# Optimization experiments

Hardware: AMD Instinct MI355X
Metric: run time of the kernel (lower is better)

The kernel has to match this reference:

```python
import jax, jax.numpy as jnp
import numpy as np

B, N, C, D = 1, 8192, 256, 128
MASK_VAL = jnp.float32(-1e16)


def setup_inputs() -> dict:
    key = jax.random.key(0)
    k_in, k_g, k_w, k_b = jax.random.split(key, 4)
    inputs = jax.random.normal(k_in, (B, N, C), dtype=jnp.float32)
    # row has at least one unmasked entry (standard GAT practice).
    graph = (jax.random.uniform(k_g, (N, N)) < 0.01).astype(jnp.float32)
    graph = jnp.maximum(graph, jnp.eye(N, dtype=jnp.float32))
    W = jax.random.normal(k_w, (D, C), dtype=jnp.float32)  # nn.Linear weight [out,in]
    b = jax.random.normal(k_b, (D,), dtype=jnp.float32)
    return {"inputs": inputs, "graph": graph, "W": W, "b": b}


def reference(inputs, graph, W, b):
    # h = W(inputs): [B,N,D]
    h = jnp.einsum('bnc,dc->bnd', inputs, W)
    # dense scores masked by adjacency: [B,N,N]
    scores = jnp.einsum('bnd,bmd->bnm', h, h) * graph[None, :, :]
    # torch: masked_fill_(scores == 0, -1e16)
    scores = jnp.where(scores == 0.0, MASK_VAL, scores)
    attention = jax.nn.softmax(scores, axis=2)
    return jnp.einsum('bnm,bmd->bnd', attention, h) + b
```

## Files before the change

### kernel.cpp

```cpp
#include <hip/hip_runtime.h>
#include <math.h>

#define Nn 8192
#define Cc 256
#define Dd 128
#define CAP 192

typedef float fx4 __attribute__((ext_vector_type(4)));

__global__ __launch_bounds__(256) void wt_kernel(const float* __restrict__ W,
                                                 float4* __restrict__ WT) {
  const int t = blockIdx.x * 256 + threadIdx.x;
  const int c4 = t >> 7;
  const int d  = t & 127;
  const float4 v = *(const float4*)(W + (size_t)d * Cc + c4 * 4);
  WT[c4 * Dd + d] = v;
}

__global__ __launch_bounds__(256) void h_kernel(const float* __restrict__ x,
                                                const float4* __restrict__ WT,
                                                float* __restrict__ h) {
  const int tid = threadIdx.x;
  const int d = tid & 127;
  const int g = tid >> 7;
  const int r0 = blockIdx.x * 16 + g * 8;
  const float4* x4 = (const float4*)(x + (size_t)r0 * Cc);

  float acc[8];
#pragma unroll
  for (int r = 0; r < 8; ++r) acc[r] = 0.f;

#pragma unroll 4
  for (int c4 = 0; c4 < Cc / 4; ++c4) {
    const float4 w = WT[c4 * Dd + d];
#pragma unroll
    for (int r = 0; r < 8; ++r) {
      const float4 u = x4[r * (Cc / 4) + c4];
      acc[r] += u.x * w.x + u.y * w.y + u.z * w.z + u.w * w.w;
    }
  }
#pragma unroll
  for (int r = 0; r < 8; ++r) {
    h[(size_t)(r0 + r) * Dd + d] = acc[r];
  }
}

__global__ __launch_bounds__(256, 4) void gat_fused(const float* __restrict__ graph,
                                                    const float* __restrict__ h,
                                                    const float* __restrict__ bias,
                                                    float* __restrict__ out) {
  __shared__ int idxs[4][CAP];
  const int wv   = threadIdx.x >> 6;
  const int lane = threadIdx.x & 63;
  const int q    = lane >> 4;
  const int ql   = lane & 15;
  const int i = blockIdx.x * 4 + wv;
  int* idx = idxs[wv];

  const float4 hiA = *(const float4*)(h + (size_t)i * Dd + ql * 8);
  const float4 hiB = *(const float4*)(h + (size_t)i * Dd + ql * 8 + 4);

  const fx4* row = (const fx4*)(graph + (size_t)i * Nn);
  const unsigned long long lmask = (1ull << lane) - 1ull;
  int cnt = 0;

  fx4 v[8];
#pragma unroll
  for (int t = 0; t < 8; ++t)
    v[t] = __builtin_nontemporal_load(&row[t * 64 + lane]);

#pragma unroll
  for (int c = 0; c < 4; ++c) {
#pragma unroll
    for (int t = 0; t < 8; ++t) {
      const fx4 cur = v[t];
      if (c < 3)
        v[t] = __builtin_nontemporal_load(&row[(c + 1) * 8 * 64 + t * 64 + lane]);
      const int col = 4 * ((c * 8 + t) * 64 + lane);
      {
        const unsigned long long mk = __ballot(cur.x != 0.f);
        if (mk) {
          const int p = cnt + __popcll(mk & lmask);
          if (cur.x != 0.f && p < CAP) idx[p] = col + 0;
          cnt += __popcll(mk);
        }
      }
      {
        const unsigned long long mk = __ballot(cur.y != 0.f);
        if (mk) {
          const int p = cnt + __popcll(mk & lmask);
          if (cur.y != 0.f && p < CAP) idx[p] = col + 1;
          cnt += __popcll(mk);
        }
      }
      {
        const unsigned long long mk = __ballot(cur.z != 0.f);
        if (mk) {
          const int p = cnt + __popcll(mk & lmask);
          if (cur.z != 0.f && p < CAP) idx[p] = col + 2;
          cnt += __popcll(mk);
        }
      }
      {
        const unsigned long long mk = __ballot(cur.w != 0.f);
        if (mk) {
          const int p = cnt + __popcll(mk & lmask);
          if (cur.w != 0.f && p < CAP) idx[p] = col + 3;
          cnt += __popcll(mk);
        }
      }
    }
  }
  const int m = min(cnt, CAP);

  float M = -INFINITY, L = 0.f;
  float4 accA = {0.f, 0.f, 0.f, 0.f};
  float4 accB = {0.f, 0.f, 0.f, 0.f};

  const int nsteps = (m + 3) >> 2;
  const int nb = (nsteps + 1) >> 1;

  float4 hvA[2], hvB[2];
#pragma unroll
  for (int u = 0; u < 2; ++u) {
    const int e = u * 4 + q;
    const int j = (e < m) ? idx[e] : i;
    hvA[u] = *(const float4*)(h + (size_t)j * Dd + ql * 8);
    hvB[u] = *(const float4*)(h + (size_t)j * Dd + ql * 8 + 4);
  }

  for (int b = 0; b < nb; ++b) {
    float4 nA[2], nB[2];
    if (b + 1 < nb) {
#pragma unroll
      for (int u = 0; u < 2; ++u) {
        const int e = (2 * (b + 1) + u) * 4 + q;
        const int j = (e < m) ? idx[e] : i;
        nA[u] = *(const float4*)(h + (size_t)j * Dd + ql * 8);
        nB[u] = *(const float4*)(h + (size_t)j * Dd + ql * 8 + 4);
      }
    }
    float sv[2];
#pragma unroll
    for (int u = 0; u < 2; ++u) {
      float pd = hiA.x * hvA[u].x + hiA.y * hvA[u].y + hiA.z * hvA[u].z + hiA.w * hvA[u].w
               + hiB.x * hvB[u].x + hiB.y * hvB[u].y + hiB.z * hvB[u].z + hiB.w * hvB[u].w;
#pragma unroll
      for (int off = 8; off > 0; off >>= 1) pd += __shfl_xor(pd, off);
      sv[u] = pd;
    }
#pragma unroll
    for (int u = 0; u < 2; ++u) {
      const int e = (2 * b + u) * 4 + q;
      const float s = (e < m) ? sv[u] : 0.f;
      if (s != 0.f) {
        const float newM = fmaxf(M, s);
        const float scale = __expf(M - newM);
        const float p = __expf(s - newM);
        L = L * scale + p;
        accA.x = accA.x * scale + p * hvA[u].x;
        accA.y = accA.y * scale + p * hvA[u].y;
        accA.z = accA.z * scale + p * hvA[u].z;
        accA.w = accA.w * scale + p * hvA[u].w;
        accB.x = accB.x * scale + p * hvB[u].x;
        accB.y = accB.y * scale + p * hvB[u].y;
        accB.z = accB.z * scale + p * hvB[u].z;
        accB.w = accB.w * scale + p * hvB[u].w;
        M = newM;
      }
    }
#pragma unroll
    for (int u = 0; u < 2; ++u) { hvA[u] = nA[u]; hvB[u] = nB[u]; }
  }

#pragma unroll
  for (int off = 16; off <= 32; off <<= 1) {
    const float Mo = __shfl_xor(M, off);
    const float Lo = __shfl_xor(L, off);
    float4 aAo, aBo;
    aAo.x = __shfl_xor(accA.x, off); aAo.y = __shfl_xor(accA.y, off);
    aAo.z = __shfl_xor(accA.z, off); aAo.w = __shfl_xor(accA.w, off);
    aBo.x = __shfl_xor(accB.x, off); aBo.y = __shfl_xor(accB.y, off);
    aBo.z = __shfl_xor(accB.z, off); aBo.w = __shfl_xor(accB.w, off);
    const float Mm = fmaxf(M, Mo);
    const float s0 = (M  > -INFINITY) ? __expf(M  - Mm) : 0.f;
    const float s1 = (Mo > -INFINITY) ? __expf(Mo - Mm) : 0.f;
    L = L * s0 + Lo * s1;
    accA.x = accA.x * s0 + aAo.x * s1;  accA.y = accA.y * s0 + aAo.y * s1;
    accA.z = accA.z * s0 + aAo.z * s1;  accA.w = accA.w * s0 + aAo.w * s1;
    accB.x = accB.x * s0 + aBo.x * s1;  accB.y = accB.y * s0 + aBo.y * s1;
    accB.z = accB.z * s0 + aBo.z * s1;  accB.w = accB.w * s0 + aBo.w * s1;
    M = Mm;
  }
  const float inv = 1.f / L;

  if (q == 0) {
    const float4 bA = *(const float4*)(bias + ql * 8);
    const float4 bB = *(const float4*)(bias + ql * 8 + 4);
    float4 oA, oB;
    oA.x = accA.x * inv + bA.x;  oA.y = accA.y * inv + bA.y;
    oA.z = accA.z * inv + bA.z;  oA.w = accA.w * inv + bA.w;
    oB.x = accB.x * inv + bB.x;  oB.y = accB.y * inv + bB.y;
    oB.z = accB.z * inv + bB.z;  oB.w = accB.w * inv + bB.w;
    *(float4*)(out + (size_t)i * Dd + ql * 8)     = oA;
    *(float4*)(out + (size_t)i * Dd + ql * 8 + 4) = oB;
  }
}

extern "C" void kernel_launch(void* const* d_in, const int* in_sizes, int n_in,
                              void* d_out, int out_size, void* d_ws, size_t ws_size,
                              hipStream_t stream) {
  const float* x     = (const float*)d_in[0];
  const float* graph = (const float*)d_in[1];
  const float* W     = (const float*)d_in[2];
  const float* bias  = (const float*)d_in[3];
  float* out = (float*)d_out;

  float*  h  = (float*)d_ws;
  float4* WT = (float4*)((char*)d_ws + (16u << 20));

  wt_kernel<<<32, 256, 0, stream>>>(W, WT);
  h_kernel<<<Nn / 16, 256, 0, stream>>>(x, WT, h);
  gat_fused<<<Nn / 4, 256, 0, stream>>>(graph, h, bias, out);
}
```

Measured before the change: 403.3 us.

## Process two rows per wave and overlap gather-softmax of row A with row B's scan

Each wavefront now handles two graph rows. While it scans and compacts the second row's adjacency, it interleaves the online-softmax gather steps for the first row, so that row's latency-bound h gathers hide under the streaming graph loads. The grid is halved to match. This trades away the previous two-step software prefetch in the gather loop and adds register pressure, which may reduce occupancy.

```diff
diff --git a/kernel.cpp b/kernel.cpp
--- a/kernel.cpp
+++ b/kernel.cpp
@@ -45,134 +45,47 @@
   }
 }
 
-__global__ __launch_bounds__(256, 4) void gat_fused(const float* __restrict__ graph,
-                                                    const float* __restrict__ h,
-                                                    const float* __restrict__ bias,
-                                                    float* __restrict__ out) {
-  __shared__ int idxs[4][CAP];
-  const int wv   = threadIdx.x >> 6;
-  const int lane = threadIdx.x & 63;
-  const int q    = lane >> 4;
-  const int ql   = lane & 15;
-  const int i = blockIdx.x * 4 + wv;
-  int* idx = idxs[wv];
-
-  const float4 hiA = *(const float4*)(h + (size_t)i * Dd + ql * 8);
-  const float4 hiB = *(const float4*)(h + (size_t)i * Dd + ql * 8 + 4);
-
-  const fx4* row = (const fx4*)(graph + (size_t)i * Nn);
-  const unsigned long long lmask = (1ull << lane) - 1ull;
-  int cnt = 0;
-
-  fx4 v[8];
-#pragma unroll
-  for (int t = 0; t < 8; ++t)
-    v[t] = __builtin_nontemporal_load(&row[t * 64 + lane]);
-
-#pragma unroll
-  for (int c = 0; c < 4; ++c) {
-#pragma unroll
-    for (int t = 0; t < 8; ++t) {
-      const fx4 cur = v[t];
-      if (c < 3)
-        v[t] = __builtin_nontemporal_load(&row[(c + 1) * 8 * 64 + t * 64 + lane]);
-      const int col = 4 * ((c * 8 + t) * 64 + lane);
-      {
-        const unsigned long long mk = __ballot(cur.x != 0.f);
-        if (mk) {
-          const int p = cnt + __popcll(mk & lmask);
-          if (cur.x != 0.f && p < CAP) idx[p] = col + 0;
-          cnt += __popcll(mk);
-        }
-      }
-      {
-        const unsigned long long mk = __ballot(cur.y != 0.f);
-        if (mk) {
-          const int p = cnt + __popcll(mk & lmask);
-          if (cur.y != 0.f && p < CAP) idx[p] = col + 1;
-          cnt += __popcll(mk);
-        }
-      }
-      {
-        const unsigned long long mk = __ballot(cur.z != 0.f);
-        if (mk) {
-          const int p = cnt + __popcll(mk & lmask);
-          if (cur.z != 0.f && p < CAP) idx[p] = col + 2;
-          cnt += __popcll(mk);
-        }
-      }
-      {
-        const unsigned long long mk = __ballot(cur.w != 0.f);
-        if (mk) {
-          const int p = cnt + __popcll(mk & lmask);
-          if (cur.w != 0.f && p < CAP) idx[p] = col + 3;
-          cnt += __popcll(mk);
-        }
-      }
-    }
-  }
-  const int m = min(cnt, CAP);
-
-  float M = -INFINITY, L = 0.f;
-  float4 accA = {0.f, 0.f, 0.f, 0.f};
-  float4 accB = {0.f, 0.f, 0.f, 0.f};
-
-  const int nsteps = (m + 3) >> 2;
-  const int nb = (nsteps + 1) >> 1;
-
-  float4 hvA[2], hvB[2];
-#pragma unroll
-  for (int u = 0; u < 2; ++u) {
-    const int e = u * 4 + q;
-    const int j = (e < m) ? idx[e] : i;
-    hvA[u] = *(const float4*)(h + (size_t)j * Dd + ql * 8);
-    hvB[u] = *(const float4*)(h + (size_t)j * Dd + ql * 8 + 4);
-  }
-
-  for (int b = 0; b < nb; ++b) {
-    float4 nA[2], nB[2];
-    if (b + 1 < nb) {
-#pragma unroll
-      for (int u = 0; u < 2; ++u) {
-        const int e = (2 * (b + 1) + u) * 4 + q;
-        const int j = (e < m) ? idx[e] : i;
-        nA[u] = *(const float4*)(h + (size_t)j * Dd + ql * 8);
-        nB[u] = *(const float4*)(h + (size_t)j * Dd + ql * 8 + 4);
-      }
-    }
-    float sv[2];
-#pragma unroll
-    for (int u = 0; u < 2; ++u) {
-      float pd = hiA.x * hvA[u].x + hiA.y * hvA[u].y + hiA.z * hvA[u].z + hiA.w * hvA[u].w
-               + hiB.x * hvB[u].x + hiB.y * hvB[u].y + hiB.z * hvB[u].z + hiB.w * hvB[u].w;
-#pragma unroll
-      for (int off = 8; off > 0; off >>= 1) pd += __shfl_xor(pd, off);
-      sv[u] = pd;
-    }
-#pragma unroll
-    for (int u = 0; u < 2; ++u) {
-      const int e = (2 * b + u) * 4 + q;
-      const float s = (e < m) ? sv[u] : 0.f;
-      if (s != 0.f) {
-        const float newM = fmaxf(M, s);
-        const float scale = __expf(M - newM);
-        const float p = __expf(s - newM);
-        L = L * scale + p;
-        accA.x = accA.x * scale + p * hvA[u].x;
-        accA.y = accA.y * scale + p * hvA[u].y;
-        accA.z = accA.z * scale + p * hvA[u].z;
-        accA.w = accA.w * scale + p * hvA[u].w;
-        accB.x = accB.x * scale + p * hvB[u].x;
-        accB.y = accB.y * scale + p * hvB[u].y;
-        accB.z = accB.z * scale + p * hvB[u].z;
-        accB.w = accB.w * scale + p * hvB[u].w;
-        M = newM;
-      }
-    }
-#pragma unroll
-    for (int u = 0; u < 2; ++u) { hvA[u] = nA[u]; hvB[u] = nB[u]; }
-  }
-
+#define COMPACT(comp, cidx)                                             \
+  {                                                                     \
+    const unsigned long long mk = __ballot((comp) != 0.f);              \
+    if (mk) {                                                           \
+      const int p = cnt + __popcll(mk & lmask);                         \
+      if ((comp) != 0.f && p < CAP) idx[p] = col + (cidx);              \
+      cnt += __popcll(mk);                                              \
+    }                                                                   \
+  }
+
+__device__ __forceinline__ void tail_step(int s, int m, const int* idx, int i,
+                                          const float* __restrict__ h,
+                                          int q, int ql,
+                                          const float4& hiA, const float4& hiB,
+                                          float& M, float& L,
+                                          float4& accA, float4& accB) {
+  const int e = s * 4 + q;
+  const int j = (e < m) ? idx[e] : i;
+  const float4 hvA = *(const float4*)(h + (size_t)j * Dd + ql * 8);
+  const float4 hvB = *(const float4*)(h + (size_t)j * Dd + ql * 8 + 4);
+  float pd = hiA.x * hvA.x + hiA.y * hvA.y + hiA.z * hvA.z + hiA.w * hvA.w
+           + hiB.x * hvB.x + hiB.y * hvB.y + hiB.z * hvB.z + hiB.w * hvB.w;
+#pragma unroll
+  for (int off = 8; off > 0; off >>= 1) pd += __shfl_xor(pd, off);
+  const float sc = (e < m) ? pd : 0.f;
+  if (sc != 0.f) {
+    const float newM = fmaxf(M, sc);
+    const float scale = __expf(M - newM);
+    const float p = __expf(sc - newM);
+    L = L * scale + p;
+    accA.x = accA.x * scale + p * hvA.x;  accA.y = accA.y * scale + p * hvA.y;
+    accA.z = accA.z * scale + p * hvA.z;  accA.w = accA.w * scale + p * hvA.w;
+    accB.x = accB.x * scale + p * hvB.x;  accB.y = accB.y * scale + p * hvB.y;
+    accB.z = accB.z * scale + p * hvB.z;  accB.w = accB.w * scale + p * hvB.w;
+    M = newM;
+  }
+}
+
+__device__ __forceinline__ void merge_write(int i, const float* __restrict__ bias,
+                                            float* __restrict__ out, int q, int ql,
+                                            float M, float L, float4 accA, float4 accB) {
 #pragma unroll
   for (int off = 16; off <= 32; off <<= 1) {
     const float Mo = __shfl_xor(M, off);
@@ -193,7 +106,6 @@
     M = Mm;
   }
   const float inv = 1.f / L;
-
   if (q == 0) {
     const float4 bA = *(const float4*)(bias + ql * 8);
     const float4 bB = *(const float4*)(bias + ql * 8 + 4);
@@ -207,6 +119,93 @@
   }
 }
 
+__global__ __launch_bounds__(256, 4) void gat_fused(const float* __restrict__ graph,
+                                                    const float* __restrict__ h,
+                                                    const float* __restrict__ bias,
+                                                    float* __restrict__ out) {
+  __shared__ int idxs[8][CAP];
+  const int wv   = threadIdx.x >> 6;
+  const int lane = threadIdx.x & 63;
+  const int q    = lane >> 4;
+  const int ql   = lane & 15;
+  const int iA = blockIdx.x * 8 + wv * 2;
+  const int iB = iA + 1;
+  int* idxA = idxs[wv * 2];
+  int* idxB = idxs[wv * 2 + 1];
+  const unsigned long long lmask = (1ull << lane) - 1ull;
+
+  const float4 hiA_A = *(const float4*)(h + (size_t)iA * Dd + ql * 8);
+  const float4 hiB_A = *(const float4*)(h + (size_t)iA * Dd + ql * 8 + 4);
+  const float4 hiA_B = *(const float4*)(h + (size_t)iB * Dd + ql * 8);
+  const float4 hiB_B = *(const float4*)(h + (size_t)iB * Dd + ql * 8 + 4);
+
+  int mA;
+  {
+    const fx4* row = (const fx4*)(graph + (size_t)iA * Nn);
+    int* idx = idxA;
+    int cnt = 0;
+    fx4 v[8];
+#pragma unroll
+    for (int t = 0; t < 8; ++t)
+      v[t] = __builtin_nontemporal_load(&row[t * 64 + lane]);
+#pragma unroll
+    for (int c = 0; c < 4; ++c) {
+#pragma unroll
+      for (int t = 0; t < 8; ++t) {
+        const fx4 cur = v[t];
+        if (c < 3)
+          v[t] = __builtin_nontemporal_load(&row[(c + 1) * 8 * 64 + t * 64 + lane]);
+        const int col = 4 * ((c * 8 + t) * 64 + lane);
+        COMPACT(cur.x, 0) COMPACT(cur.y, 1) COMPACT(cur.z, 2) COMPACT(cur.w, 3)
+      }
+    }
+    mA = min(cnt, CAP);
+  }
+
+  float MA = -INFINITY, LA = 0.f;
+  float4 accA_A = {0.f, 0.f, 0.f, 0.f}, accB_A = {0.f, 0.f, 0.f, 0.f};
+  int sA = 0;
+  const int nsA = (mA + 3) >> 2;
+
+  int mB;
+  {
+    const fx4* row = (const fx4*)(graph + (size_t)iB * Nn);
+    int* idx = idxB;
+    int cnt = 0;
+    fx4 v[8];
+#pragma unroll
+    for (int t = 0; t < 8; ++t)
+      v[t] = __builtin_nontemporal_load(&row[t * 64 + lane]);
+#pragma unroll
+    for (int c = 0; c < 4; ++c) {
+#pragma unroll
+      for (int t = 0; t < 8; ++t) {
+        const fx4 cur = v[t];
+        if (c < 3)
+          v[t] = __builtin_nontemporal_load(&row[(c + 1) * 8 * 64 + t * 64 + lane]);
+        const int col = 4 * ((c * 8 + t) * 64 + lane);
+        COMPACT(cur.x, 0) COMPACT(cur.y, 1) COMPACT(cur.z, 2) COMPACT(cur.w, 3)
+        if (sA < nsA) {
+          tail_step(sA, mA, idxA, iA, h, q, ql, hiA_A, hiB_A, MA, LA, accA_A, accB_A);
+          ++sA;
+        }
+      }
+    }
+    mB = min(cnt, CAP);
+  }
+
+  for (; sA < nsA; ++sA)
+    tail_step(sA, mA, idxA, iA, h, q, ql, hiA_A, hiB_A, MA, LA, accA_A, accB_A);
+  merge_write(iA, bias, out, q, ql, MA, LA, accA_A, accB_A);
+
+  float MB = -INFINITY, LB = 0.f;
+  float4 accA_B = {0.f, 0.f, 0.f, 0.f}, accB_B = {0.f, 0.f, 0.f, 0.f};
+  const int nsB = (mB + 3) >> 2;
+  for (int s = 0; s < nsB; ++s)
+    tail_step(s, mB, idxB, iB, h, q, ql, hiA_B, hiB_B, MB, LB, accA_B, accB_B);
+  merge_write(iB, bias, out, q, ql, MB, LB, accA_B, accB_B);
+}
+
 extern "C" void kernel_launch(void* const* d_in, const int* in_sizes, int n_in,
                               void* d_out, int out_size, void* d_ws, size_t ws_size,
                               hipStream_t stream) {
@@ -221,5 +220,5 @@
 
   wt_kernel<<<32, 256, 0, stream>>>(W, WT);
   h_kernel<<<Nn / 16, 256, 0, stream>>>(x, WT, h);
-  gat_fused<<<Nn / 4, 256, 0, stream>>>(graph, h, bias, out);
-}
+  gat_fused<<<Nn / 8, 256, 0, stream>>>(graph, h, bias, out);
+}
```

Measured after the change: 410.9 us. No clear change (+1.9%).
